# Kernel optimization log

Measured on AMD Instinct MI355X. Metric: run time of the kernel, lower is better.

Reference implementation:

```python
import jax, jax.numpy as jnp
import numpy as np

B, H, S, D = 2, 16, 2048, 64
DILATION_RATE = 2

def dilated_global_mask(seq_len: int, dilation_rate: int) -> jnp.ndarray:
    # mask[i, j] = 1 if |i - j| % dilation_rate == 0 else 0  -> [S, S] float32
    i = jnp.arange(seq_len)[:, None]
    j = jnp.arange(seq_len)[None, :]
    return ((jnp.abs(i - j) % dilation_rate) == 0).astype(jnp.float32)

def setup_inputs() -> dict:
    key = jax.random.key(0)
    kq, kk, kv = jax.random.split(key, 3)
    queries = jax.random.normal(kq, (B, H, S, D), dtype=jnp.float32)
    keys = jax.random.normal(kk, (B, H, S, D), dtype=jnp.float32)
    values = jax.random.normal(kv, (B, H, S, D), dtype=jnp.float32)
    return {"queries": queries, "keys": keys, "values": values}

def reference(queries, keys, values):
    depth = queries.shape[-1]
    # scores: [B, H, S, S]
    scores = jnp.einsum("bhqd,bhkd->bhqk", queries, keys)
    scores = scores / jnp.sqrt(jnp.asarray(depth, dtype=jnp.float32))
    gmask = dilated_global_mask(keys.shape[-2], DILATION_RATE)  # [S, S]
    # NOTE: multiplicative masking (masked scores become 0, not -inf), as in source
    masked_scores = scores * gmask
    attention_probs = jax.nn.softmax(masked_scores, axis=-1)
    # dropout is identity at inference (training=None)
    out = jnp.einsum("bhqk,bhkd->bhqd", attention_probs, values)
    return out
```

## Files before the change

### kernel.cpp

```cpp
#include <hip/hip_runtime.h>
#include <hip/hip_bf16.h>


#define B_   2
#define H_   16
#define S_   2048
#define D_   64
#define SP_  1024
#define BQ   64
#define BK   64
#define NKT  (SP_ / BK)
#define LSTR 72

#define QSCALE 0.180336884f

typedef __bf16 bf16x8 __attribute__((ext_vector_type(8)));
typedef float  f32x4  __attribute__((ext_vector_type(4)));

__global__ __launch_bounds__(256) void vsum_kernel(const float* __restrict__ V,
                                                   float* __restrict__ vsum) {
    const int bh  = blockIdx.x >> 3;
    const int c   = blockIdx.x & 7;
    const int tid = threadIdx.x;
    const int d   = tid & 63;
    const int rq  = tid >> 6;
    const float* p0 = V + (size_t)bh * S_ * D_ + (size_t)(c * 256 + rq * 64) * D_ + d;
    float se = 0.f, so = 0.f;
    for (int j = 0; j < 64; j += 2) {
        se += p0[(size_t)j * D_];
        so += p0[(size_t)(j + 1) * D_];
    }
    __shared__ float red[2][4][64];
    red[0][rq][d] = se;
    red[1][rq][d] = so;
    __syncthreads();
    if (tid < 128) {
        const int p = tid >> 6, dd = tid & 63;
        const float s = red[p][0][dd] + red[p][1][dd] + red[p][2][dd] + red[p][3][dd];
        atomicAdd(&vsum[((size_t)bh * 2 + p) * D_ + dd], s);
    }
}

__global__ __launch_bounds__(256, 4) void attn_kernel(const float* __restrict__ Q,
                                                      const float* __restrict__ K,
                                                      const float* __restrict__ V,
                                                      const float* __restrict__ vsum,
                                                      float* __restrict__ out) {
    const int bh  = blockIdx.x;
    const int par = blockIdx.y;
    const int qt  = blockIdx.z;
    const int tid  = threadIdx.x;
    const int lane = tid & 63;
    const int wave = tid >> 6;
    const int l15  = lane & 15;
    const int quad = lane >> 4;

    __shared__ __align__(16) __bf16 q_s[BQ][LSTR];
    __shared__ __align__(16) __bf16 k_s[BK][LSTR];
    __shared__ __align__(16) __bf16 v_s[D_][LSTR];
    __shared__ __align__(16) __bf16 p_s[4][16][64];

    const size_t base = (size_t)bh * S_ * D_;
    const float* Qb = Q + base;
    const float* Kb = K + base;
    const float* Vb = V + base;

    #pragma unroll
    for (int i = 0; i < 2; ++i) {
        const int f = (i << 8) + tid;
        const int r = f >> 3, c8 = f & 7;
        const float* src = Qb + (size_t)(par + 2 * (qt * BQ + r)) * D_ + c8 * 8;
        const float4 a = *(const float4*)src;
        const float4 b = *(const float4*)(src + 4);
        bf16x8 w;
        w[0] = (__bf16)(a.x * QSCALE); w[1] = (__bf16)(a.y * QSCALE);
        w[2] = (__bf16)(a.z * QSCALE); w[3] = (__bf16)(a.w * QSCALE);
        w[4] = (__bf16)(b.x * QSCALE); w[5] = (__bf16)(b.y * QSCALE);
        w[6] = (__bf16)(b.z * QSCALE); w[7] = (__bf16)(b.w * QSCALE);
        *(bf16x8*)&q_s[r][c8 * 8] = w;
    }

    f32x4 acc[4];
    #pragma unroll
    for (int nt = 0; nt < 4; ++nt) acc[nt] = (f32x4){0.f, 0.f, 0.f, 0.f};
    float l_acc[4] = {0.f, 0.f, 0.f, 0.f};

    const int q0 = wave * 16;

    for (int kt = 0; kt < NKT; ++kt) {
        __syncthreads();

        #pragma unroll
        for (int i = 0; i < 2; ++i) {
            const int f = (i << 8) + tid;
            const int r = f >> 3, c8 = f & 7;
            const float* src = Kb + (size_t)(par + 2 * (kt * BK + r)) * D_ + c8 * 8;
            const float4 a = *(const float4*)src;
            const float4 b = *(const float4*)(src + 4);
            bf16x8 w;
            w[0] = (__bf16)a.x; w[1] = (__bf16)a.y; w[2] = (__bf16)a.z; w[3] = (__bf16)a.w;
            w[4] = (__bf16)b.x; w[5] = (__bf16)b.y; w[6] = (__bf16)b.z; w[7] = (__bf16)b.w;
            *(bf16x8*)&k_s[r][c8 * 8] = w;
        }
        #pragma unroll
        for (int i = 0; i < 2; ++i) {
            const int r0 = (wave + 4 * i) << 3;
            const float* src = Vb + (size_t)(par + 2 * (kt * BK + r0)) * D_ + lane;
            bf16x8 w;
            #pragma unroll
            for (int j = 0; j < 8; ++j)
                w[j] = (__bf16)src[(size_t)(2 * j) * D_];
            *(bf16x8*)&v_s[lane][r0] = w;
        }
        __syncthreads();

        f32x4 sc[4];
        #pragma unroll
        for (int nt = 0; nt < 4; ++nt) sc[nt] = (f32x4){0.f, 0.f, 0.f, 0.f};
        #pragma unroll
        for (int ks = 0; ks < 2; ++ks) {
            const bf16x8 a = *(const bf16x8*)&q_s[q0 + l15][ks * 32 + quad * 8];
            #pragma unroll
            for (int nt = 0; nt < 4; ++nt) {
                const bf16x8 b = *(const bf16x8*)&k_s[nt * 16 + l15][ks * 32 + quad * 8];
                sc[nt] = __builtin_amdgcn_mfma_f32_16x16x32_bf16(a, b, sc[nt], 0, 0, 0);
            }
        }

        #pragma unroll
        for (int nt = 0; nt < 4; ++nt) {
            const int colw = ((((nt + quad) & 3) << 4) + l15);
            #pragma unroll
            for (int r = 0; r < 4; ++r) {
                const float p = exp2f(sc[nt][r]);
                l_acc[r] += p;
                p_s[wave][quad * 4 + r][colw] = (__bf16)p;
            }
        }

        #pragma unroll
        for (int ks = 0; ks < 2; ++ks) {
            const int col0 = ((((2 * ks + (quad >> 1) + (l15 >> 2)) & 3) << 4)
                              + ((quad & 1) << 3));
            const bf16x8 pa = *(const bf16x8*)&p_s[wave][l15][col0];
            #pragma unroll
            for (int nt = 0; nt < 4; ++nt) {
                const bf16x8 bv = *(const bf16x8*)&v_s[nt * 16 + l15][ks * 32 + quad * 8];
                acc[nt] = __builtin_amdgcn_mfma_f32_16x16x32_bf16(pa, bv, acc[nt], 0, 0, 0);
            }
        }
    }

    float rz[4];
    #pragma unroll
    for (int r = 0; r < 4; ++r) {
        float s = l_acc[r];
        #pragma unroll
        for (int off = 1; off < 16; off <<= 1) s += __shfl_xor(s, off);
        rz[r] = 1.0f / (s + 1024.0f);
    }
    const float* vs_o = vsum + ((size_t)bh * 2 + (1 - par)) * D_;
    #pragma unroll
    for (int nt = 0; nt < 4; ++nt) {
        const float vso = vs_o[nt * 16 + l15];
        #pragma unroll
        for (int r = 0; r < 4; ++r) {
            const int qg = par + 2 * (qt * BQ + q0 + quad * 4 + r);
            out[base + (size_t)qg * D_ + nt * 16 + l15] = (acc[nt][r] + vso) * rz[r];
        }
    }
}

extern "C" void kernel_launch(void* const* d_in, const int* in_sizes, int n_in,
                              void* d_out, int out_size, void* d_ws, size_t ws_size,
                              hipStream_t stream) {
    const float* Q = (const float*)d_in[0];
    const float* K = (const float*)d_in[1];
    const float* V = (const float*)d_in[2];
    float* out  = (float*)d_out;
    float* vsum = (float*)d_ws;

    hipMemsetAsync(vsum, 0, (size_t)B_ * H_ * 2 * D_ * sizeof(float), stream);
    vsum_kernel<<<dim3(B_ * H_ * 8), dim3(256), 0, stream>>>(V, vsum);
    attn_kernel<<<dim3(B_ * H_, 2, SP_ / BQ), dim3(256), 0, stream>>>(Q, K, V, vsum, out);
}
```

Baseline: 130.7 us.

## Fuse opposite-parity V sum into attention kernel and register-prefetch K/V tiles

Removes the separate memset and vsum kernel. Each attention block now accumulates the opposite-parity V column sums itself, reading the neighbouring row alongside each V load and reducing them through shared memory at the end. It also prefetches the next K/V tile into registers while the MFMA work on the current tile runs, which moves one barrier to the end of each iteration. This cuts two launches but makes every block redundantly read the other half of V and raises register pressure.

```diff
diff --git a/kernel.cpp b/kernel.cpp
--- a/kernel.cpp
+++ b/kernel.cpp
@@ -17,34 +17,9 @@
 typedef __bf16 bf16x8 __attribute__((ext_vector_type(8)));
 typedef float  f32x4  __attribute__((ext_vector_type(4)));
 
-__global__ __launch_bounds__(256) void vsum_kernel(const float* __restrict__ V,
-                                                   float* __restrict__ vsum) {
-    const int bh  = blockIdx.x >> 3;
-    const int c   = blockIdx.x & 7;
-    const int tid = threadIdx.x;
-    const int d   = tid & 63;
-    const int rq  = tid >> 6;
-    const float* p0 = V + (size_t)bh * S_ * D_ + (size_t)(c * 256 + rq * 64) * D_ + d;
-    float se = 0.f, so = 0.f;
-    for (int j = 0; j < 64; j += 2) {
-        se += p0[(size_t)j * D_];
-        so += p0[(size_t)(j + 1) * D_];
-    }
-    __shared__ float red[2][4][64];
-    red[0][rq][d] = se;
-    red[1][rq][d] = so;
-    __syncthreads();
-    if (tid < 128) {
-        const int p = tid >> 6, dd = tid & 63;
-        const float s = red[p][0][dd] + red[p][1][dd] + red[p][2][dd] + red[p][3][dd];
-        atomicAdd(&vsum[((size_t)bh * 2 + p) * D_ + dd], s);
-    }
-}
-
 __global__ __launch_bounds__(256, 4) void attn_kernel(const float* __restrict__ Q,
                                                       const float* __restrict__ K,
                                                       const float* __restrict__ V,
-                                                      const float* __restrict__ vsum,
                                                       float* __restrict__ out) {
     const int bh  = blockIdx.x;
     const int par = blockIdx.y;
@@ -59,11 +34,13 @@
     __shared__ __align__(16) __bf16 k_s[BK][LSTR];
     __shared__ __align__(16) __bf16 v_s[D_][LSTR];
     __shared__ __align__(16) __bf16 p_s[4][16][64];
+    __shared__ float vo_red[4][64];
 
     const size_t base = (size_t)bh * S_ * D_;
     const float* Qb = Q + base;
     const float* Kb = K + base;
     const float* Vb = V + base;
+    const int vofs = (par == 0) ? D_ : -D_;
 
     #pragma unroll
     for (int i = 0; i < 2; ++i) {
@@ -80,39 +57,65 @@
         *(bf16x8*)&q_s[r][c8 * 8] = w;
     }
 
+    float4 pk[2][2];
+    float  pv[2][8], pvo[2][8];
+
+    auto issue_loads = [&](int kt) {
+        #pragma unroll
+        for (int i = 0; i < 2; ++i) {
+            const int f = (i << 8) + tid;
+            const int r = f >> 3, c8 = f & 7;
+            const float* ksrc = Kb + (size_t)(par + 2 * (kt * BK + r)) * D_ + c8 * 8;
+            pk[i][0] = *(const float4*)ksrc;
+            pk[i][1] = *(const float4*)(ksrc + 4);
+        }
+        #pragma unroll
+        for (int i = 0; i < 2; ++i) {
+            const int r0 = (wave + 4 * i) << 3;
+            const float* vsrc = Vb + (size_t)(par + 2 * (kt * BK + r0)) * D_ + lane;
+            #pragma unroll
+            for (int j = 0; j < 8; ++j) {
+                pv[i][j]  = vsrc[(size_t)(2 * j) * D_];
+                pvo[i][j] = vsrc[(size_t)(2 * j) * D_ + vofs];
+            }
+        }
+    };
+
+    issue_loads(0);
+
     f32x4 acc[4];
     #pragma unroll
     for (int nt = 0; nt < 4; ++nt) acc[nt] = (f32x4){0.f, 0.f, 0.f, 0.f};
     float l_acc[4] = {0.f, 0.f, 0.f, 0.f};
+    float vo = 0.f;
 
     const int q0 = wave * 16;
 
     for (int kt = 0; kt < NKT; ++kt) {
-        __syncthreads();
-
         #pragma unroll
         for (int i = 0; i < 2; ++i) {
             const int f = (i << 8) + tid;
             const int r = f >> 3, c8 = f & 7;
-            const float* src = Kb + (size_t)(par + 2 * (kt * BK + r)) * D_ + c8 * 8;
-            const float4 a = *(const float4*)src;
-            const float4 b = *(const float4*)(src + 4);
             bf16x8 w;
-            w[0] = (__bf16)a.x; w[1] = (__bf16)a.y; w[2] = (__bf16)a.z; w[3] = (__bf16)a.w;
-            w[4] = (__bf16)b.x; w[5] = (__bf16)b.y; w[6] = (__bf16)b.z; w[7] = (__bf16)b.w;
+            w[0] = (__bf16)pk[i][0].x; w[1] = (__bf16)pk[i][0].y;
+            w[2] = (__bf16)pk[i][0].z; w[3] = (__bf16)pk[i][0].w;
+            w[4] = (__bf16)pk[i][1].x; w[5] = (__bf16)pk[i][1].y;
+            w[6] = (__bf16)pk[i][1].z; w[7] = (__bf16)pk[i][1].w;
             *(bf16x8*)&k_s[r][c8 * 8] = w;
         }
         #pragma unroll
         for (int i = 0; i < 2; ++i) {
             const int r0 = (wave + 4 * i) << 3;
-            const float* src = Vb + (size_t)(par + 2 * (kt * BK + r0)) * D_ + lane;
             bf16x8 w;
             #pragma unroll
-            for (int j = 0; j < 8; ++j)
-                w[j] = (__bf16)src[(size_t)(2 * j) * D_];
+            for (int j = 0; j < 8; ++j) w[j] = (__bf16)pv[i][j];
             *(bf16x8*)&v_s[lane][r0] = w;
+            vo += ((pvo[i][0] + pvo[i][1]) + (pvo[i][2] + pvo[i][3]))
+                + ((pvo[i][4] + pvo[i][5]) + (pvo[i][6] + pvo[i][7]));
         }
         __syncthreads();
+
+        if (kt + 1 < NKT) issue_loads(kt + 1);
 
         f32x4 sc[4];
         #pragma unroll
@@ -149,7 +152,11 @@
                 acc[nt] = __builtin_amdgcn_mfma_f32_16x16x32_bf16(pa, bv, acc[nt], 0, 0, 0);
             }
         }
+        __syncthreads();
     }
+
+    vo_red[wave][lane] = vo;
+    __syncthreads();
 
     float rz[4];
     #pragma unroll
@@ -159,14 +166,14 @@
         for (int off = 1; off < 16; off <<= 1) s += __shfl_xor(s, off);
         rz[r] = 1.0f / (s + 1024.0f);
     }
-    const float* vs_o = vsum + ((size_t)bh * 2 + (1 - par)) * D_;
     #pragma unroll
     for (int nt = 0; nt < 4; ++nt) {
-        const float vso = vs_o[nt * 16 + l15];
+        const int d = nt * 16 + l15;
+        const float vso = (vo_red[0][d] + vo_red[1][d]) + (vo_red[2][d] + vo_red[3][d]);
         #pragma unroll
         for (int r = 0; r < 4; ++r) {
             const int qg = par + 2 * (qt * BQ + q0 + quad * 4 + r);
-            out[base + (size_t)qg * D_ + nt * 16 + l15] = (acc[nt][r] + vso) * rz[r];
+            out[base + (size_t)qg * D_ + d] = (acc[nt][r] + vso) * rz[r];
         }
     }
 }
@@ -177,10 +184,6 @@
     const float* Q = (const float*)d_in[0];
     const float* K = (const float*)d_in[1];
     const float* V = (const float*)d_in[2];
-    float* out  = (float*)d_out;
-    float* vsum = (float*)d_ws;
-
-    hipMemsetAsync(vsum, 0, (size_t)B_ * H_ * 2 * D_ * sizeof(float), stream);
-    vsum_kernel<<<dim3(B_ * H_ * 8), dim3(256), 0, stream>>>(V, vsum);
-    attn_kernel<<<dim3(B_ * H_, 2, SP_ / BQ), dim3(256), 0, stream>>>(Q, K, V, vsum, out);
+    float* out = (float*)d_out;
+    attn_kernel<<<dim3(B_ * H_, 2, SP_ / BQ), dim3(256), 0, stream>>>(Q, K, V, out);
 }
```

New measurement: 139.5 us. 6.8% more time.
